# Kernel optimization log

Hardware: AMD Instinct MI355X
Metric: run time of the kernel (lower is better)

The kernel has to match this reference:

```python
import jax, jax.numpy as jnp
import numpy as np

B, S, T = 64, 64, 20
E, H, V, K = 512, 1024, 32000, 100
L, W = 50, 8
NEG = -1e9


def lstm_cell(x, h, c, Wih, Whh, bih, bhh):
    # PyTorch gate order: input, forget, cell, output
    g = x @ Wih.T + h @ Whh.T + bih + bhh
    i, f, gg, o = jnp.split(g, 4, axis=-1)
    c = jax.nn.sigmoid(f) * c + jax.nn.sigmoid(i) * jnp.tanh(gg)
    h = jax.nn.sigmoid(o) * jnp.tanh(c)
    return h, c


def setup_inputs():
    key = jax.random.key(0)
    ks = jax.random.split(key, 32)
    rn = lambda k, shp, s=0.02: (s * jax.random.normal(k, shp)).astype(jnp.float32)
    embed_W = jax.random.normal(ks[0], (V, E), dtype=jnp.float32).at[0].set(0.0)  # padding_idx 0
    return {
        'src_seqs': jax.random.randint(ks[1], (B, S), 1, V),
        'src_lengths': jax.random.randint(ks[2], (B,), S // 2, S + 1),
        'trg_seqs': jax.random.randint(ks[3], (B, T), 1, V),
        'ctc_seqs': jax.random.randint(ks[4], (B, L, W), 1, V),
        'ctc_lengths': jax.random.randint(ks[5], (B,), 1, L + 1),
        'embed_W': embed_W,
        'enc_Wih': rn(ks[6], (4 * H, E)), 'enc_Whh': rn(ks[7], (4 * H, H)),
        'enc_bih': rn(ks[8], (4 * H,)), 'enc_bhh': rn(ks[9], (4 * H,)),
        'dec_Wih': rn(ks[10], (4 * H, E + H)), 'dec_Whh': rn(ks[11], (4 * H, H)),
        'dec_bih': rn(ks[12], (4 * H,)), 'dec_bhh': rn(ks[13], (4 * H,)),
        'qk_W': rn(ks[14], (K, E)), 'qk_b': rn(ks[15], (K,)),
        'qv_W': rn(ks[16], (H, E)), 'qv_b': rn(ks[17], (H,)),
        'ak_W': rn(ks[18], (K, H)), 'ak_b': rn(ks[19], (K,)),
        'out_W': rn(ks[20], (E, 2 * H)), 'out_b': rn(ks[21], (E,)),
        'wd_b': rn(ks[22], (V,)),
        'hf1_W': rn(ks[23], (2 * H, H)), 'hf1_b': rn(ks[24], (2 * H,)),
        'hf2_W': rn(ks[25], (H, 2 * H)), 'hf2_b': rn(ks[26], (H,)),
        'cf1_W': rn(ks[27], (2 * H, H)), 'cf1_b': rn(ks[28], (2 * H,)),
        'cf2_W': rn(ks[29], (H, 2 * H)), 'cf2_b': rn(ks[30], (H,)),
    }


def forward(floats, ints):
    (embed_W, enc_Wih, enc_Whh, enc_bih, enc_bhh, dec_Wih, dec_Whh, dec_bih, dec_bhh,
     qk_W, qk_b, qv_W, qv_b, ak_W, ak_b, out_W, out_b, wd_b,
     hf1_W, hf1_b, hf2_W, hf2_b, cf1_W, cf1_b, cf2_W, cf2_b) = floats
    src_seqs, src_lengths, trg_seqs, ctc_seqs, ctc_lengths = ints

    src_embed = embed_W[src_seqs]  # [B,S,E]

    # ---- encoder LSTM (seq-first scan); packed-seq final state = state at src_lengths-1 ----
    def enc_step(carry, x_t):
        h, c = lstm_cell(x_t, carry[0], carry[1], enc_Wih, enc_Whh, enc_bih, enc_bhh)
        return (h, c), (h, c)
    z = jnp.zeros((B, H), jnp.float32)
    _, (hs, cs) = jax.lax.scan(enc_step, (z, z), src_embed.transpose(1, 0, 2))  # [S,B,H]
    idx = src_lengths - 1
    h_last = hs[idx, jnp.arange(B)]
    c_last = cs[idx, jnp.arange(B)]

    # ---- init_hidden: MLP transforms of encoder final state ----
    h0 = jax.nn.relu(h_last @ hf1_W.T + hf1_b) @ hf2_W.T + hf2_b
    c0 = jax.nn.relu(c_last @ cf1_W.T + cf1_b) @ cf2_W.T + cf2_b

    # ---- persona context: mean word embedding per context item ----
    ctx_embed = embed_W[ctc_seqs].mean(axis=2)       # [B,L,E]
    q_key = jnp.tanh(ctx_embed @ qk_W.T + qk_b)      # [B,L,K]
    q_value = ctx_embed @ qv_W.T + qv_b              # [B,L,H]
    mask = jnp.arange(L)[None, :] < ctc_lengths[:, None]  # [B,L]

    ans_embed = embed_W[trg_seqs]                    # [B,T,E]

    # ---- decoder: per-step attention + LSTM + tied-vocab projection ----
    def dec_step(carry, x_t):
        h, c = carry
        a_key = jnp.tanh(h @ ak_W.T + ak_b)                      # [B,K]
        e = jnp.einsum('blk,bk->bl', q_key, a_key)
        w = jax.nn.softmax(jnp.where(mask, e, NEG), axis=1)
        ctx = jnp.einsum('bl,blh->bh', w, q_value)               # [B,H]
        h, c = lstm_cell(jnp.concatenate([x_t, ctx], -1), h, c,
                         dec_Wih, dec_Whh, dec_bih, dec_bhh)
        ox = jnp.concatenate([h, ctx], -1) @ out_W.T + out_b     # [B,E]
        logits = ox @ embed_W.T + wd_b                           # tied weights, [B,V]
        return (h, c), logits

    # teacher forcing (sampling_rate=1.0, T-1 <= max_len-2)
    _, logits = jax.lax.scan(dec_step, (h0, c0), ans_embed[:, :T - 1].transpose(1, 0, 2))
    return logits.transpose(1, 0, 2)  # [B, T-1, V]


def reference(src_seqs, src_lengths, trg_seqs, ctc_seqs, ctc_lengths, embed_W, enc_Wih, enc_Whh, enc_bih, enc_bhh, dec_Wih, dec_Whh, dec_bih, dec_bhh, qk_W, qk_b, qv_W, qv_b, ak_W, ak_b, out_W, out_b, wd_b, hf1_W, hf1_b, hf2_W, hf2_b, cf1_W, cf1_b, cf2_W, cf2_b):
    floats = (embed_W, enc_Wih, enc_Whh, enc_bih, enc_bhh, dec_Wih, dec_Whh, dec_bih, dec_bhh,
              qk_W, qk_b, qv_W, qv_b, ak_W, ak_b, out_W, out_b, wd_b,
              hf1_W, hf1_b, hf2_W, hf2_b, cf1_W, cf1_b, cf2_W, cf2_b)
    ints = (src_seqs, src_lengths, trg_seqs, ctc_seqs, ctc_lengths)
    return forward(floats, ints)
```

## Files before the change

### kernel.cpp

```cpp
#include <hip/hip_runtime.h>
#include <hip/hip_bf16.h>
#include <math.h>

#define Bn 64
#define Sn 64
#define Tn 20
#define TD 19
#define En 512
#define Hn 1024
#define Vn 32000
#define Kan 100
#define Lnn 50
#define Wnn 8

typedef __attribute__((ext_vector_type(8))) short short8v;
typedef __attribute__((ext_vector_type(4))) float floatx4;
typedef __hip_bfloat16 bf16;
typedef unsigned long long ull;

__device__ __forceinline__ float sigm(float x) { return 1.0f / (1.0f + expf(-x)); }
__device__ __forceinline__ float bfb2f(unsigned int u) {
    return __builtin_bit_cast(float, u << 16);
}
__device__ __forceinline__ unsigned short f2bfb(float f) {
    return __builtin_bit_cast(unsigned short, __float2bfloat16(f));
}

#define ALOAD(p)     __hip_atomic_load((p), __ATOMIC_RELAXED, __HIP_MEMORY_SCOPE_AGENT)
#define ASTORE(p, v) __hip_atomic_store((p), (v), __ATOMIC_RELAXED, __HIP_MEMORY_SCOPE_AGENT)

__device__ __forceinline__ uint4 aload16(const ull* base, int ullIdx) {
    ull u0 = ALOAD(base + ullIdx);
    ull u1 = ALOAD(base + ullIdx + 1);
    uint4 v;
    v.x = (unsigned)u0; v.y = (unsigned)(u0 >> 32);
    v.z = (unsigned)u1; v.w = (unsigned)(u1 >> 32);
    return v;
}

__device__ __forceinline__ uint4 gload16(const void* p) {
    uint4 v;
    asm volatile("global_load_dwordx4 %0, %1, off sc0 sc1"
                 : "=v"(v) : "v"(p));
    return v;
}
#define GWAIT() asm volatile("s_waitcnt vmcnt(0)" ::: "memory")

__device__ __forceinline__ void gbar(unsigned int* c, int tid) {
    __builtin_amdgcn_sched_barrier(0);
    __syncthreads();
    if (tid == 0) {
        __hip_atomic_fetch_add(c, 1u, __ATOMIC_RELAXED, __HIP_MEMORY_SCOPE_AGENT);
        while (__hip_atomic_load(c, __ATOMIC_RELAXED, __HIP_MEMORY_SCOPE_AGENT) < 128u) {
            __builtin_amdgcn_s_sleep(1);
        }
    }
    __syncthreads();
    __builtin_amdgcn_sched_barrier(0);
}

#define EOFF(r, p) (((r) << 5) + ((((p) ^ ((r) & 3))) << 3))

__device__ __forceinline__ int aswz(int row, int p) {
    return row * 32 + (((p ^ ((row >> 1) & 3))) << 3);
}
__device__ __forceinline__ int wswz(int col, int s, int K) {
    return col * K + (((s & ~7) | ((s & 7) ^ (col & 7))) << 3);
}

template<int GATHER, int EPI, int ACT>
__global__ __launch_bounds__(256)
void mgemm(const bf16* __restrict__ A, int lda, const int* __restrict__ tok,
           const bf16* __restrict__ W, int ldw,
           const float* __restrict__ b1, const float* __restrict__ b2,
           float* __restrict__ C, int ldc,
           bf16* __restrict__ Cbf, int ldcbf,
           int M, int N, int K)
{
    __shared__ bf16 As[128 * 32];
    __shared__ bf16 Bs[128 * 32];
    const int tid = threadIdx.x;
    const int lane = tid & 63, wv = tid >> 6;
    const int wm = wv >> 1, wn = wv & 1;
    const int n0 = (EPI == 2 ? blockIdx.y : blockIdx.x) * 128;
    const int r0 = (EPI == 2 ? blockIdx.x : blockIdx.y) * 128;
    const int srow = tid >> 2, sp = tid & 3;

    const int ra_r0 = r0 + srow, ra_r1 = r0 + srow + 64;
    const bool av0 = ra_r0 < M, av1 = ra_r1 < M;
    const size_t arow0 = (size_t)(av0 ? (GATHER ? tok[ra_r0] : ra_r0) : 0) * lda;
    const size_t arow1 = (size_t)(av1 ? (GATHER ? tok[ra_r1] : ra_r1) : 0) * lda;
    const size_t wrow0 = (size_t)(n0 + srow) * ldw;
    const size_t wrow1 = (size_t)(n0 + srow + 64) * ldw;

    const uint4 z4 = make_uint4(0, 0, 0, 0);
    uint4 ra0, ra1, rb0, rb1;
#define LOADTILE_G(k0) do { \
        ra0 = av0 ? *((const uint4*)(A + arow0 + (k0)) + sp) : z4; \
        ra1 = av1 ? *((const uint4*)(A + arow1 + (k0)) + sp) : z4; \
        rb0 = *((const uint4*)(W + wrow0 + (k0)) + sp); \
        rb1 = *((const uint4*)(W + wrow1 + (k0)) + sp); \
    } while (0)

    floatx4 acc[4][4] = {};
    const int lr = lane & 15, p2 = lane >> 4;

    LOADTILE_G(0);
    for (int k0 = 0; k0 < K; k0 += 32) {
        __syncthreads();
        *(uint4*)(As + EOFF(srow, sp)) = ra0;
        *(uint4*)(As + EOFF(srow + 64, sp)) = ra1;
        *(uint4*)(Bs + EOFF(srow, sp)) = rb0;
        *(uint4*)(Bs + EOFF(srow + 64, sp)) = rb1;
        __syncthreads();
        if (k0 + 32 < K) LOADTILE_G(k0 + 32);
        short8v aF[4], bF[4];
#pragma unroll
        for (int mf = 0; mf < 4; ++mf)
            aF[mf] = *(const short8v*)(As + EOFF(wm * 64 + mf * 16 + lr, p2));
#pragma unroll
        for (int nf = 0; nf < 4; ++nf)
            bF[nf] = *(const short8v*)(Bs + EOFF(wn * 64 + nf * 16 + lr, p2));
#pragma unroll
        for (int mf = 0; mf < 4; ++mf)
#pragma unroll
            for (int nf = 0; nf < 4; ++nf)
                acc[mf][nf] = __builtin_amdgcn_mfma_f32_16x16x32_bf16(
                    aF[mf], bF[nf], acc[mf][nf], 0, 0, 0);
    }
#undef LOADTILE_G

    const int rbase = r0 + wm * 64 + (lane >> 4) * 4;
    const int nbase = n0 + wn * 64 + (lane & 15);
#pragma unroll
    for (int nf = 0; nf < 4; ++nf) {
        const int n = nbase + nf * 16;
        if (n >= N) continue;
        float bias = b1 ? b1[n] : 0.0f;
        if (b2) bias += b2[n];
#pragma unroll
        for (int mf = 0; mf < 4; ++mf) {
#pragma unroll
            for (int i = 0; i < 4; ++i) {
                const int r = rbase + mf * 16 + i;
                if (r >= M) continue;
                float v = acc[mf][nf][i] + bias;
                if (ACT == 1) v = tanhf(v);
                if (ACT == 2) v = fmaxf(v, 0.0f);
                if (EPI == 2) {
                    int b = r & 63, t = r >> 6;
                    C[(size_t)(b * TD + t) * Vn + n] = v;
                } else {
                    if (C) C[(size_t)r * ldc + n] = v;
                    if (Cbf) Cbf[(size_t)r * ldcbf + n] = __float2bfloat16(v);
                }
            }
        }
    }
}

struct EncP {
    const bf16* Wp;
    const bf16* Xg;
    bf16* hA; bf16* hB;
    const int* len;
    bf16* hlast; bf16* clast;
    unsigned int* cnt;
};

__global__ __launch_bounds__(512, 1)
void enc_persist(EncP p)
{
    __shared__ bf16 Ws_l[32 * 1024];
    __shared__ bf16 Asb[2][64 * 32];
    __shared__ float Gs[64][33];
    const int tid = threadIdx.x;
    const int lane = tid & 63, wv = tid >> 6;
    const int mf = wv >> 1, nf = wv & 1;
    const int blk = blockIdx.x;
    const int n0 = blk * 32;

    for (int idx = tid; idx < 32 * 128; idx += 512) {
        int col = idx >> 7, s = idx & 127;
        uint4 v = *(const uint4*)(p.Wp + (size_t)(n0 + col) * 1024 + s * 8);
        *(uint4*)(Ws_l + wswz(col, s, 1024)) = v;
    }

    const int b = tid >> 3, jl = tid & 7;
    const int j = (n0 >> 2) + jl;
    float c_reg = 0.0f;
    const int hw = b * 256 + blk * 2 + (jl >> 2);
    if ((lane & 3) == 0) ASTORE((ull*)p.hA + hw, 0ull);
    const int mylen = p.len[b];

    const int arow = mf * 16 + (lane & 15);
    const int a_rd = aswz(arow, lane >> 4);
    const int bcol = nf * 16 + (lane & 15);
    const int bbase = bcol * 1024;
    const int srow = tid >> 2, sp = tid & 3;
    const int a_wr = aswz(srow, sp);
    const int gr = mf * 16 + (lane >> 4) * 4;
    const int gc = nf * 16 + (lane & 15);

    gbar(p.cnt + 0, tid);

    for (int t = 0; t < Sn; ++t) {
        const bf16* hsrc = (t & 1) ? p.hB : p.hA;
        bf16* hn = (t & 1) ? p.hA : p.hB;
        const bf16* hrow = hsrc + srow * 1024 + sp * 8;
        const bf16* xg = p.Xg + ((size_t)t * Bn + b) * 4096;
        float xf0 = __bfloat162float(xg[j]);
        float xf1 = __bfloat162float(xg[1024 + j]);
        float xf2 = __bfloat162float(xg[2048 + j]);
        float xf3 = __bfloat162float(xg[3072 + j]);
        floatx4 acc = {};
        uint4 ra;
        if (tid < 256) ra = gload16(hrow);
        __syncthreads();
        if (tid < 256) { GWAIT(); *(uint4*)(Asb[0] + a_wr) = ra; }
        if (tid < 256) ra = gload16(hrow + 32);
        for (int k0 = 0; k0 < 1024; k0 += 32) {
            const int cur = (k0 >> 5) & 1;
            __syncthreads();
            if (k0 + 32 < 1024) {
                if (tid < 256) { GWAIT(); *(uint4*)(Asb[cur ^ 1] + a_wr) = ra; }
                if (k0 + 64 < 1024 && tid < 256)
                    ra = gload16(hrow + k0 + 64);
            }
            short8v af = *(const short8v*)(Asb[cur] + a_rd);
            int s = (k0 >> 3) + (lane >> 4);
            short8v bfr = *(const short8v*)(Ws_l + bbase +
                             (((s & ~7) | ((s & 7) ^ (bcol & 7))) << 3));
            acc = __builtin_amdgcn_mfma_f32_16x16x32_bf16(af, bfr, acc, 0, 0, 0);
        }
        Gs[gr + 0][gc] = acc[0];
        Gs[gr + 1][gc] = acc[1];
        Gs[gr + 2][gc] = acc[2];
        Gs[gr + 3][gc] = acc[3];
        __syncthreads();
        float gi = Gs[b][jl * 4 + 0] + xf0;
        float gf = Gs[b][jl * 4 + 1] + xf1;
        float gg = Gs[b][jl * 4 + 2] + xf2;
        float go = Gs[b][jl * 4 + 3] + xf3;
        float cnv = sigm(gf) * c_reg + sigm(gi) * tanhf(gg);
        float hnv = sigm(go) * tanhf(cnv);
        c_reg = cnv;
        if (t == mylen - 1) {
            p.hlast[b * 1024 + j] = __float2bfloat16(hnv);
            p.clast[b * 1024 + j] = __float2bfloat16(cnv);
        }
        {
            unsigned int q0 = f2bfb(hnv);
            unsigned int q1 = __shfl_down(q0, 1);
            unsigned int q2 = __shfl_down(q0, 2);
            unsigned int q3 = __shfl_down(q0, 3);
            if ((lane & 3) == 0)
                ASTORE((ull*)hn + hw,
                       (ull)q0 | ((ull)q1 << 16) | ((ull)q2 << 32) | ((ull)q3 << 48));
        }
        if (t < Sn - 1) gbar(p.cnt + 1 + t, tid);
    }
}

struct DecP {
    const bf16* Wp;
    const bf16* Xg;
    bf16* hA; bf16* hB;
    bf16* ctx;
    const float* c0;
    const float* akW; const float* akb;
    const float* qkey;
    const float* qval;
    const int* clen;
    bf16* hcat;
    unsigned int* cnt;
};

__global__ __launch_bounds__(512, 1)
void dec_persist(DecP p)
{
    __shared__ bf16 Ws_l[32 * 2048];
    __shared__ bf16 Asb[2][64 * 32];
    __shared__ float Gs[64][33];
    __shared__ float akey[104];
    __shared__ float ebuf[52];
    __shared__ float wts[52];
    float* hsh = &Gs[0][0];

    const int tid = threadIdx.x;
    const int lane = tid & 63, wv = tid >> 6;
    const int mf = wv >> 1, nf = wv & 1;
    const int blk = blockIdx.x;
    const int n0 = blk * 32;

    for (int idx = tid; idx < 32 * 256; idx += 512) {
        int col = idx >> 8, s = idx & 255;
        uint4 v = *(const uint4*)(p.Wp + (size_t)(n0 + col) * 2048 + s * 8);
        *(uint4*)(Ws_l + wswz(col, s, 2048)) = v;
    }

    const int b = tid >> 3, jl = tid & 7;
    const int j = (n0 >> 2) + jl;
    float c_reg = p.c0[b * 1024 + j];
    const int hw = b * 256 + blk * 2 + (jl >> 2);

    const int arow = mf * 16 + (lane & 15);
    const int a_rd = aswz(arow, lane >> 4);
    const int bcol = nf * 16 + (lane & 15);
    const int bbase = bcol * 2048;
    const int srow = tid >> 2, sp = tid & 3;
    const int a_wr = aswz(srow, sp);
    const int gr = mf * 16 + (lane >> 4) * 4;
    const int gc = nf * 16 + (lane & 15);
    const int sbase = srow * 256 + sp * 2;

    gbar(p.cnt + 64, tid);

    for (int t = 0; t < TD; ++t) {
        const bf16* hsrc = (t & 1) ? p.hB : p.hA;
        bf16* hn = (t & 1) ? p.hA : p.hB;
        const ull* hq = (const ull*)hsrc;
        const ull* cq = (const ull*)p.ctx;
        unsigned int* ctxc = p.cnt + 90 + t;

        if (blk < 64) {
            const int ab = blk;
            if (tid < 256) {
                ull v = ALOAD(hq + ab * 256 + tid);
                hsh[tid * 4 + 0] = bfb2f((unsigned)(v & 0xffff));
                hsh[tid * 4 + 1] = bfb2f((unsigned)((v >> 16) & 0xffff));
                hsh[tid * 4 + 2] = bfb2f((unsigned)((v >> 32) & 0xffff));
                hsh[tid * 4 + 3] = bfb2f((unsigned)(v >> 48));
            }
            __syncthreads();
            for (int k = wv; k < Kan; k += 8) {
                float s = 0.0f;
#pragma unroll
                for (int m = 0; m < 16; ++m)
                    s += hsh[lane + m * 64] * p.akW[(size_t)k * 1024 + lane + m * 64];
                for (int off = 32; off; off >>= 1) s += __shfl_down(s, off);
                if (lane == 0) akey[k] = tanhf(s + p.akb[k]);
            }
            __syncthreads();
            for (int l = wv; l < Lnn; l += 8) {
                const float* qr = p.qkey + (size_t)(ab * Lnn + l) * Kan;
                float s = qr[lane] * akey[lane];
                if (lane < Kan - 64) s += qr[lane + 64] * akey[lane + 64];
                for (int off = 32; off; off >>= 1) s += __shfl_down(s, off);
                if (lane == 0) ebuf[l] = s;
            }
            __syncthreads();
            if (wv == 0) {
                int len = p.clen[ab];
                float e = (lane < Lnn) ? (lane < len ? ebuf[lane] : -1e9f)
                                       : -3.402823466e38f;
                float mx = e;
                for (int off = 32; off; off >>= 1) mx = fmaxf(mx, __shfl_xor(mx, off));
                float pr = (lane < Lnn) ? expf(e - mx) : 0.0f;
                float sm = pr;
                for (int off = 32; off; off >>= 1) sm += __shfl_xor(sm, off);
                if (lane < Lnn) wts[lane] = pr / sm;
            }
            __syncthreads();
#pragma unroll
            for (int pass = 0; pass < 2; ++pass) {
                int jj = tid + pass * 512;
                const float* qv = p.qval + (size_t)ab * Lnn * 1024 + jj;
                float s0 = 0.0f, s1 = 0.0f;
                for (int l = 0; l < Lnn; l += 2) {
                    s0 += wts[l] * qv[(size_t)l * 1024];
                    s1 += wts[l + 1] * qv[(size_t)(l + 1) * 1024];
                }
                unsigned short cb = f2bfb(s0 + s1);
                p.hcat[((size_t)t * Bn + ab) * 2048 + 1024 + jj] =
                    __builtin_bit_cast(bf16, cb);
                unsigned int q0 = cb;
                unsigned int q1 = __shfl_down(q0, 1);
                unsigned int q2 = __shfl_down(q0, 2);
                unsigned int q3 = __shfl_down(q0, 3);
                if ((lane & 3) == 0)
                    ASTORE((ull*)p.ctx + ab * 256 + pass * 128 + (tid >> 2),
                           (ull)q0 | ((ull)q1 << 16) | ((ull)q2 << 32) | ((ull)q3 << 48));
            }
            __syncthreads();
            if (tid == 0)
                __hip_atomic_fetch_add(ctxc, 1u, __ATOMIC_RELAXED,
                                       __HIP_MEMORY_SCOPE_AGENT);
        }

        const bf16* xg = p.Xg + ((size_t)t * Bn + b) * 4096;
        float xf0 = __bfloat162float(xg[j]);
        float xf1 = __bfloat162float(xg[1024 + j]);
        float xf2 = __bfloat162float(xg[2048 + j]);
        float xf3 = __bfloat162float(xg[3072 + j]);
        floatx4 acc = {};
        uint4 ra;
        if (tid < 256) ra = aload16(hq, sbase);
        __syncthreads();
        if (tid < 256) *(uint4*)(Asb[0] + a_wr) = ra;
        if (tid < 256) ra = aload16(hq, sbase + 8);
        for (int i = 0; i < 64; ++i) {
            if (i == 30) {
                __builtin_amdgcn_sched_barrier(0);
                if (tid == 0) {
                    while (__hip_atomic_load(ctxc, __ATOMIC_RELAXED,
                                             __HIP_MEMORY_SCOPE_AGENT) < 64u) {
                        __builtin_amdgcn_s_sleep(1);
                    }
                }
                __syncthreads();
                __builtin_amdgcn_sched_barrier(0);
            }
            __syncthreads();
            if (i + 1 < 64 && tid < 256) {
                *(uint4*)(Asb[(i + 1) & 1] + a_wr) = ra;
                if (i + 2 < 64) {
                    const ull* aq = (i + 2 < 32) ? hq : cq;
                    ra = aload16(aq, sbase + (((i + 2) & 31) << 3));
                }
            }
            short8v af = *(const short8v*)(Asb[i & 1] + a_rd);
            int s = 4 * i + (lane >> 4);
            short8v bfr = *(const short8v*)(Ws_l + bbase +
                             (((s & ~7) | ((s & 7) ^ (bcol & 7))) << 3));
            acc = __builtin_amdgcn_mfma_f32_16x16x32_bf16(af, bfr, acc, 0, 0, 0);
        }
        Gs[gr + 0][gc] = acc[0];
        Gs[gr + 1][gc] = acc[1];
        Gs[gr + 2][gc] = acc[2];
        Gs[gr + 3][gc] = acc[3];
        __syncthreads();
        float gi = Gs[b][jl * 4 + 0] + xf0;
        float gf = Gs[b][jl * 4 + 1] + xf1;
        float gg = Gs[b][jl * 4 + 2] + xf2;
        float go = Gs[b][jl * 4 + 3] + xf3;
        float cnv = sigm(gf) * c_reg + sigm(gi) * tanhf(gg);
        float hnv = sigm(go) * tanhf(cnv);
        c_reg = cnv;
        bf16 hb = __float2bfloat16(hnv);
        p.hcat[((size_t)t * Bn + b) * 2048 + j] = hb;
        {
            unsigned int q0 = f2bfb(hnv);
            unsigned int q1 = __shfl_down(q0, 1);
            unsigned int q2 = __shfl_down(q0, 2);
            unsigned int q3 = __shfl_down(q0, 3);
            if ((lane & 3) == 0)
                ASTORE((ull*)hn + hw,
                       (ull)q0 | ((ull)q1 << 16) | ((ull)q2 << 32) | ((ull)q3 << 48));
        }
        if (t < TD - 1) gbar(p.cnt + 65 + t, tid);
    }
}

__global__ __launch_bounds__(128)
void ctx_embed_kernel(const int* __restrict__ ctc, const float* __restrict__ embed,
                      bf16* __restrict__ ctxe_bf)
{
    const int row = blockIdx.x;
    const int tid = threadIdx.x;
    __shared__ int toks[8];
    if (tid < 8) toks[tid] = ctc[row * Wnn + tid];
    __syncthreads();
#pragma unroll
    for (int p = 0; p < 4; ++p) {
        int e = tid + p * 128;
        float s = 0.0f;
#pragma unroll
        for (int w = 0; w < 8; ++w) s += embed[(size_t)toks[w] * En + e];
        ctxe_bf[(size_t)row * En + e] = __float2bfloat16(s * 0.125f);
    }
}

__global__ void prep_tokens(const int* __restrict__ src, const int* __restrict__ trg,
                            int* __restrict__ tokA, int* __restrict__ tokD)
{
    int i = blockIdx.x * 256 + threadIdx.x;
    if (i < Bn * Sn) tokA[i] = src[(i & 63) * Sn + (i >> 6)];
    if (i < TD * Bn) tokD[i] = trg[(i & 63) * Tn + (i >> 6)];
}

__global__ void conv_f2b(const float* __restrict__ src, bf16* __restrict__ dst, int n)
{
    int i = (blockIdx.x * 256 + threadIdx.x) * 4;
    if (i >= n) return;
    float4 v = *(const float4*)(src + i);
    dst[i + 0] = __float2bfloat16(v.x);
    dst[i + 1] = __float2bfloat16(v.y);
    dst[i + 2] = __float2bfloat16(v.z);
    dst[i + 3] = __float2bfloat16(v.w);
}

__global__ void pad_qkw(const float* __restrict__ qkW, bf16* __restrict__ Wp)
{
    int i = blockIdx.x * 256 + threadIdx.x;
    int r = i >> 9;
    Wp[i] = __float2bfloat16(r < Kan ? qkW[(size_t)r * En + (i & 511)] : 0.0f);
}

__global__ void perm_enc(const float* __restrict__ Whh, bf16* __restrict__ Wp)
{
    int row = blockIdx.x;
    int j = row >> 2, g = row & 3;
    const float* s = Whh + (size_t)(g * 1024 + j) * 1024;
    bf16* d = Wp + (size_t)row * 1024;
    for (int e = threadIdx.x; e < 1024; e += 256) d[e] = __float2bfloat16(s[e]);
}

__global__ void perm_dec(const float* __restrict__ Whh, const float* __restrict__ Wih,
                         bf16* __restrict__ Wp)
{
    int row = blockIdx.x;
    int j = row >> 2, g = row & 3;
    int sr = g * 1024 + j;
    const float* s1 = Whh + (size_t)sr * 1024;
    const float* s2 = Wih + (size_t)sr * 1536 + 512;
    bf16* d = Wp + (size_t)row * 2048;
    for (int e = threadIdx.x; e < 1024; e += 256) {
        d[e] = __float2bfloat16(s1[e]);
        d[1024 + e] = __float2bfloat16(s2[e]);
    }
}

extern "C" void kernel_launch(void* const* d_in, const int* in_sizes, int n_in,
                              void* d_out, int out_size, void* d_ws, size_t ws_size,
                              hipStream_t stream)
{
    (void)in_sizes; (void)n_in; (void)out_size; (void)ws_size;
    const int*   src     = (const int*)d_in[0];
    const int*   srclen  = (const int*)d_in[1];
    const int*   trg     = (const int*)d_in[2];
    const int*   ctc     = (const int*)d_in[3];
    const int*   ctclen  = (const int*)d_in[4];
    const float* embed   = (const float*)d_in[5];
    const float* enc_Wih = (const float*)d_in[6];
    const float* enc_Whh = (const float*)d_in[7];
    const float* enc_bih = (const float*)d_in[8];
    const float* enc_bhh = (const float*)d_in[9];
    const float* dec_Wih = (const float*)d_in[10];
    const float* dec_Whh = (const float*)d_in[11];
    const float* dec_bih = (const float*)d_in[12];
    const float* dec_bhh = (const float*)d_in[13];
    const float* qkW     = (const float*)d_in[14];
    const float* qkb     = (const float*)d_in[15];
    const float* qvW     = (const float*)d_in[16];
    const float* qvb     = (const float*)d_in[17];
    const float* akW     = (const float*)d_in[18];
    const float* akb     = (const float*)d_in[19];
    const float* outW    = (const float*)d_in[20];
    const float* outb    = (const float*)d_in[21];
    const float* wdb     = (const float*)d_in[22];
    const float* hf1W    = (const float*)d_in[23];
    const float* hf1b    = (const float*)d_in[24];
    const float* hf2W    = (const float*)d_in[25];
    const float* hf2b    = (const float*)d_in[26];
    const float* cf1W    = (const float*)d_in[27];
    const float* cf1b    = (const float*)d_in[28];
    const float* cf2W    = (const float*)d_in[29];
    const float* cf2b    = (const float*)d_in[30];
    float* out = (float*)d_out;

    char* ws = (char*)d_ws;
    size_t off = 0;
    auto alloc = [&](size_t bytes) -> void* {
        void* p = ws + off;
        off += (bytes + 255) & ~(size_t)255;
        return p;
    };
    bf16*  embed_bf  = (bf16*)alloc((size_t)Vn * En * 2);
    bf16*  encWih_bf = (bf16*)alloc((size_t)4096 * En * 2);
    bf16*  decWih_bf = (bf16*)alloc((size_t)4096 * 1536 * 2);
    bf16*  qvW_bf    = (bf16*)alloc((size_t)Hn * En * 2);
    bf16*  outW_bf   = (bf16*)alloc((size_t)En * 2048 * 2);
    bf16*  Wenc_p    = (bf16*)alloc((size_t)4096 * 1024 * 2);
    bf16*  Wdec_p    = (bf16*)alloc((size_t)4096 * 2048 * 2);
    bf16*  hf1W_bf   = (bf16*)alloc((size_t)2048 * 1024 * 2);
    bf16*  hf2W_bf   = (bf16*)alloc((size_t)1024 * 2048 * 2);
    bf16*  cf1W_bf   = (bf16*)alloc((size_t)2048 * 1024 * 2);
    bf16*  cf2W_bf   = (bf16*)alloc((size_t)1024 * 2048 * 2);
    bf16*  qkWp      = (bf16*)alloc((size_t)128 * En * 2);
    bf16*  Xenc_bf   = (bf16*)alloc((size_t)Sn * Bn * 4096 * 2);
    bf16*  Xdec_bf   = (bf16*)alloc((size_t)TD * Bn * 4096 * 2);
    float* qkey      = (float*)alloc((size_t)Bn * Lnn * Kan * 4);
    float* qval      = (float*)alloc((size_t)Bn * Lnn * Hn * 4);
    bf16*  ctxe_bf   = (bf16*)alloc((size_t)Bn * Lnn * En * 2);
    bf16*  henc0     = (bf16*)alloc((size_t)Bn * Hn * 2);
    bf16*  henc1     = (bf16*)alloc((size_t)Bn * Hn * 2);
    bf16*  hdec0     = (bf16*)alloc((size_t)Bn * Hn * 2);
    bf16*  hdec1     = (bf16*)alloc((size_t)Bn * Hn * 2);
    bf16*  ctxbuf    = (bf16*)alloc((size_t)Bn * Hn * 2);
    float* cbuf0     = (float*)alloc((size_t)Bn * Hn * 4);
    bf16*  hlast_bf  = (bf16*)alloc((size_t)Bn * Hn * 2);
    bf16*  clast_bf  = (bf16*)alloc((size_t)Bn * Hn * 2);
    bf16*  t2h_bf    = (bf16*)alloc((size_t)Bn * 2048 * 2);
    bf16*  t2c_bf    = (bf16*)alloc((size_t)Bn * 2048 * 2);
    int*   tokA      = (int*)alloc((size_t)Bn * Sn * 4);
    int*   tokD      = (int*)alloc((size_t)TD * Bn * 4);
    unsigned int* cnt = (unsigned int*)alloc(128 * 4);
    bf16*  hcat_bf   = Xenc_bf;
    bf16*  ox_bf     = Xenc_bf + (size_t)TD * Bn * 2048;

    hipMemsetAsync(cnt, 0, 128 * 4, stream);

    conv_f2b<<<(Vn * En) / 1024, 256, 0, stream>>>(embed, embed_bf, Vn * En);
    conv_f2b<<<(4096 * En) / 1024, 256, 0, stream>>>(enc_Wih, encWih_bf, 4096 * En);
    conv_f2b<<<(4096 * 1536) / 1024, 256, 0, stream>>>(dec_Wih, decWih_bf, 4096 * 1536);
    conv_f2b<<<(Hn * En) / 1024, 256, 0, stream>>>(qvW, qvW_bf, Hn * En);
    conv_f2b<<<(En * 2048) / 1024, 256, 0, stream>>>(outW, outW_bf, En * 2048);
    conv_f2b<<<(2048 * 1024) / 1024, 256, 0, stream>>>(hf1W, hf1W_bf, 2048 * 1024);
    conv_f2b<<<(1024 * 2048) / 1024, 256, 0, stream>>>(hf2W, hf2W_bf, 1024 * 2048);
    conv_f2b<<<(2048 * 1024) / 1024, 256, 0, stream>>>(cf1W, cf1W_bf, 2048 * 1024);
    conv_f2b<<<(1024 * 2048) / 1024, 256, 0, stream>>>(cf2W, cf2W_bf, 1024 * 2048);
    pad_qkw<<<(128 * En) / 256, 256, 0, stream>>>(qkW, qkWp);
    perm_enc<<<4096, 256, 0, stream>>>(enc_Whh, Wenc_p);
    perm_dec<<<4096, 256, 0, stream>>>(dec_Whh, dec_Wih, Wdec_p);
    prep_tokens<<<16, 256, 0, stream>>>(src, trg, tokA, tokD);
    ctx_embed_kernel<<<Bn * Lnn, 128, 0, stream>>>(ctc, embed, ctxe_bf);

    mgemm<1, 0, 0><<<dim3(32, 32), 256, 0, stream>>>(
        embed_bf, En, tokA, encWih_bf, En, enc_bih, enc_bhh,
        nullptr, 0, Xenc_bf, 4096, Bn * Sn, 4096, En);
    mgemm<1, 0, 0><<<dim3(32, 10), 256, 0, stream>>>(
        embed_bf, En, tokD, decWih_bf, 1536, dec_bih, dec_bhh,
        nullptr, 0, Xdec_bf, 4096, TD * Bn, 4096, En);
    mgemm<0, 0, 0><<<dim3(8, 25), 256, 0, stream>>>(
        ctxe_bf, En, nullptr, qvW_bf, En, qvb, nullptr,
        qval, Hn, nullptr, 0, Bn * Lnn, Hn, En);
    mgemm<0, 0, 1><<<dim3(1, 25), 256, 0, stream>>>(
        ctxe_bf, En, nullptr, qkWp, En, qkb, nullptr,
        qkey, Kan, nullptr, 0, Bn * Lnn, Kan, En);

    {
        EncP ep;
        ep.Wp = Wenc_p; ep.Xg = Xenc_bf; ep.hA = henc0; ep.hB = henc1;
        ep.len = srclen; ep.hlast = hlast_bf; ep.clast = clast_bf; ep.cnt = cnt;
        void* args[] = {&ep};
        hipLaunchCooperativeKernel((void*)enc_persist, dim3(128), dim3(512),
                                   args, 0, stream);
    }

    mgemm<0, 0, 2><<<dim3(16, 1), 256, 0, stream>>>(
        hlast_bf, Hn, nullptr, hf1W_bf, Hn, hf1b, nullptr,
        nullptr, 0, t2h_bf, 2048, Bn, 2048, Hn);
    mgemm<0, 0, 0><<<dim3(8, 1), 256, 0, stream>>>(
        t2h_bf, 2048, nullptr, hf2W_bf, 2048, hf2b, nullptr,
        nullptr, 0, hdec0, 1024, Bn, Hn, 2048);
    mgemm<0, 0, 2><<<dim3(16, 1), 256, 0, stream>>>(
        clast_bf, Hn, nullptr, cf1W_bf, Hn, cf1b, nullptr,
        nullptr, 0, t2c_bf, 2048, Bn, 2048, Hn);
    mgemm<0, 0, 0><<<dim3(8, 1), 256, 0, stream>>>(
        t2c_bf, 2048, nullptr, cf2W_bf, 2048, cf2b, nullptr,
        cbuf0, Hn, nullptr, 0, Bn, Hn, 2048);

    {
        DecP dp;
        dp.Wp = Wdec_p; dp.Xg = Xdec_bf; dp.hA = hdec0; dp.hB = hdec1;
        dp.ctx = ctxbuf; dp.c0 = cbuf0;
        dp.akW = akW; dp.akb = akb; dp.qkey = qkey; dp.qval = qval;
        dp.clen = ctclen; dp.hcat = hcat_bf; dp.cnt = cnt;
        void* args[] = {&dp};
        hipLaunchCooperativeKernel((void*)dec_persist, dim3(128), dim3(512),
                                   args, 0, stream);
    }

    mgemm<0, 0, 0><<<dim3(4, 10), 256, 0, stream>>>(
        hcat_bf, 2048, nullptr, outW_bf, 2048, outb, nullptr,
        nullptr, 0, ox_bf, En, TD * Bn, En, 2048);
    mgemm<0, 2, 0><<<dim3(10, Vn / 128), 256, 0, stream>>>(
        ox_bf, En, nullptr, embed_bf, En, wdb, nullptr,
        out, 0, nullptr, 0, TD * Bn, Vn, En);
}
```

Before: 2.809 ms.

## Deepen encoder h prefetch ring with atomic loads; store qval as bf16

The encoder persistent kernel's recurrent-state load moves from a single in-flight inline-asm load with an explicit waitcnt to an 8-deep register ring of relaxed atomic loads. This keeps several h chunks in flight and avoids a full vmcnt(0) wait on every k-step. Separately, the attention value tensor qval is written and read as bf16 instead of fp32, halving the bytes the decoder's context reduction reads each step. The cost is more registers for the ring and reduced precision in the context values.

```diff
diff --git a/kernel.cpp b/kernel.cpp
--- a/kernel.cpp
+++ b/kernel.cpp
@@ -37,14 +37,6 @@
     v.z = (unsigned)u1; v.w = (unsigned)(u1 >> 32);
     return v;
 }
-
-__device__ __forceinline__ uint4 gload16(const void* p) {
-    uint4 v;
-    asm volatile("global_load_dwordx4 %0, %1, off sc0 sc1"
-                 : "=v"(v) : "v"(p));
-    return v;
-}
-#define GWAIT() asm volatile("s_waitcnt vmcnt(0)" ::: "memory")
 
 __device__ __forceinline__ void gbar(unsigned int* c, int tid) {
     __builtin_amdgcn_sched_barrier(0);
@@ -193,45 +185,50 @@
     if ((lane & 3) == 0) ASTORE((ull*)p.hA + hw, 0ull);
     const int mylen = p.len[b];
 
-    const int arow = mf * 16 + (lane & 15);
-    const int a_rd = aswz(arow, lane >> 4);
+    const int a_rd = aswz(mf * 16 + (lane & 15), lane >> 4);
     const int bcol = nf * 16 + (lane & 15);
     const int bbase = bcol * 1024;
     const int srow = tid >> 2, sp = tid & 3;
     const int a_wr = aswz(srow, sp);
     const int gr = mf * 16 + (lane >> 4) * 4;
     const int gc = nf * 16 + (lane & 15);
+    const int sbase = srow * 256 + sp * 2;
 
     gbar(p.cnt + 0, tid);
 
+    const int NT = 32;
     for (int t = 0; t < Sn; ++t) {
-        const bf16* hsrc = (t & 1) ? p.hB : p.hA;
+        const ull* hq = (const ull*)((t & 1) ? p.hB : p.hA);
         bf16* hn = (t & 1) ? p.hA : p.hB;
-        const bf16* hrow = hsrc + srow * 1024 + sp * 8;
         const bf16* xg = p.Xg + ((size_t)t * Bn + b) * 4096;
         float xf0 = __bfloat162float(xg[j]);
         float xf1 = __bfloat162float(xg[1024 + j]);
         float xf2 = __bfloat162float(xg[2048 + j]);
         float xf3 = __bfloat162float(xg[3072 + j]);
         floatx4 acc = {};
-        uint4 ra;
-        if (tid < 256) ra = gload16(hrow);
-        __syncthreads();
-        if (tid < 256) { GWAIT(); *(uint4*)(Asb[0] + a_wr) = ra; }
-        if (tid < 256) ra = gload16(hrow + 32);
-        for (int k0 = 0; k0 < 1024; k0 += 32) {
-            const int cur = (k0 >> 5) & 1;
-            __syncthreads();
-            if (k0 + 32 < 1024) {
-                if (tid < 256) { GWAIT(); *(uint4*)(Asb[cur ^ 1] + a_wr) = ra; }
-                if (k0 + 64 < 1024 && tid < 256)
-                    ra = gload16(hrow + k0 + 64);
-            }
-            short8v af = *(const short8v*)(Asb[cur] + a_rd);
-            int s = (k0 >> 3) + (lane >> 4);
-            short8v bfr = *(const short8v*)(Ws_l + bbase +
-                             (((s & ~7) | ((s & 7) ^ (bcol & 7))) << 3));
-            acc = __builtin_amdgcn_mfma_f32_16x16x32_bf16(af, bfr, acc, 0, 0, 0);
+        uint4 ring[8];
+        if (tid < 256) {
+#pragma unroll
+            for (int q = 0; q < 8; ++q) ring[q] = aload16(hq, sbase + q * 8);
+            *(uint4*)(Asb[0] + a_wr) = ring[0];
+            ring[0] = aload16(hq, sbase + 8 * 8);
+        }
+        for (int g = 0; g < NT / 8; ++g) {
+#pragma unroll
+            for (int u = 0; u < 8; ++u) {
+                const int i = g * 8 + u;
+                __syncthreads();
+                if (tid < 256 && i + 1 < NT) {
+                    *(uint4*)(Asb[(u + 1) & 1] + a_wr) = ring[(u + 1) & 7];
+                    if (i + 9 < NT)
+                        ring[(u + 1) & 7] = aload16(hq, sbase + (i + 9) * 8);
+                }
+                short8v af = *(const short8v*)(Asb[u & 1] + a_rd);
+                int s = 4 * i + (lane >> 4);
+                short8v bfr = *(const short8v*)(Ws_l + bbase +
+                                 (((s & ~7) | ((s & 7) ^ (bcol & 7))) << 3));
+                acc = __builtin_amdgcn_mfma_f32_16x16x32_bf16(af, bfr, acc, 0, 0, 0);
+            }
         }
         Gs[gr + 0][gc] = acc[0];
         Gs[gr + 1][gc] = acc[1];
@@ -270,7 +267,7 @@
     const float* c0;
     const float* akW; const float* akb;
     const float* qkey;
-    const float* qval;
+    const bf16* qval;
     const int* clen;
     bf16* hcat;
     unsigned int* cnt;
@@ -304,8 +301,7 @@
     float c_reg = p.c0[b * 1024 + j];
     const int hw = b * 256 + blk * 2 + (jl >> 2);
 
-    const int arow = mf * 16 + (lane & 15);
-    const int a_rd = aswz(arow, lane >> 4);
+    const int a_rd = aswz(mf * 16 + (lane & 15), lane >> 4);
     const int bcol = nf * 16 + (lane & 15);
     const int bbase = bcol * 2048;
     const int srow = tid >> 2, sp = tid & 3;
@@ -317,9 +313,8 @@
     gbar(p.cnt + 64, tid);
 
     for (int t = 0; t < TD; ++t) {
-        const bf16* hsrc = (t & 1) ? p.hB : p.hA;
+        const ull* hq = (const ull*)((t & 1) ? p.hB : p.hA);
         bf16* hn = (t & 1) ? p.hA : p.hB;
-        const ull* hq = (const ull*)hsrc;
         const ull* cq = (const ull*)p.ctx;
         unsigned int* ctxc = p.cnt + 90 + t;
 
@@ -365,11 +360,11 @@
 #pragma unroll
             for (int pass = 0; pass < 2; ++pass) {
                 int jj = tid + pass * 512;
-                const float* qv = p.qval + (size_t)ab * Lnn * 1024 + jj;
+                const bf16* qv = p.qval + (size_t)ab * Lnn * 1024 + jj;
                 float s0 = 0.0f, s1 = 0.0f;
                 for (int l = 0; l < Lnn; l += 2) {
-                    s0 += wts[l] * qv[(size_t)l * 1024];
-                    s1 += wts[l + 1] * qv[(size_t)(l + 1) * 1024];
+                    s0 += wts[l] * __bfloat162float(qv[(size_t)l * 1024]);
+                    s1 += wts[l + 1] * __bfloat162float(qv[(size_t)(l + 1) * 1024]);
                 }
                 unsigned short cb = f2bfb(s0 + s1);
                 p.hcat[((size_t)t * Bn + ab) * 2048 + 1024 + jj] =
@@ -581,7 +576,7 @@
     bf16*  Xenc_bf   = (bf16*)alloc((size_t)Sn * Bn * 4096 * 2);
     bf16*  Xdec_bf   = (bf16*)alloc((size_t)TD * Bn * 4096 * 2);
     float* qkey      = (float*)alloc((size_t)Bn * Lnn * Kan * 4);
-    float* qval      = (float*)alloc((size_t)Bn * Lnn * Hn * 4);
+    bf16*  qval_bf   = (bf16*)alloc((size_t)Bn * Lnn * Hn * 2);
     bf16*  ctxe_bf   = (bf16*)alloc((size_t)Bn * Lnn * En * 2);
     bf16*  henc0     = (bf16*)alloc((size_t)Bn * Hn * 2);
     bf16*  henc1     = (bf16*)alloc((size_t)Bn * Hn * 2);
@@ -624,7 +619,7 @@
         nullptr, 0, Xdec_bf, 4096, TD * Bn, 4096, En);
     mgemm<0, 0, 0><<<dim3(8, 25), 256, 0, stream>>>(
         ctxe_bf, En, nullptr, qvW_bf, En, qvb, nullptr,
-        qval, Hn, nullptr, 0, Bn * Lnn, Hn, En);
+        nullptr, 0, qval_bf, Hn, Bn * Lnn, Hn, En);
     mgemm<0, 0, 1><<<dim3(1, 25), 256, 0, stream>>>(
         ctxe_bf, En, nullptr, qkWp, En, qkb, nullptr,
         qkey, Kan, nullptr, 0, Bn * Lnn, Kan, En);
@@ -655,7 +650,7 @@
         DecP dp;
         dp.Wp = Wdec_p; dp.Xg = Xdec_bf; dp.hA = hdec0; dp.hB = hdec1;
         dp.ctx = ctxbuf; dp.c0 = cbuf0;
-        dp.akW = akW; dp.akb = akb; dp.qkey = qkey; dp.qval = qval;
+        dp.akW = akW; dp.akb = akb; dp.qkey = qkey; dp.qval = qval_bf;
         dp.clen = ctclen; dp.hcat = hcat_bf; dp.cnt = cnt;
         void* args[] = {&dp};
         hipLaunchCooperativeKernel((void*)dec_persist, dim3(128), dim3(512),
```

New measurement: 2.323 ms, median of 3. -17.3%, faster.
